# Optimization experiments

Measured on AMD Instinct MI355X. Metric: run time of the kernel, lower is better.

## Reference

```python
import jax, jax.numpy as jnp
import numpy as np

B, S, D, V, MAXLEN, K = 1, 2048, 768, 32000, 2048, 3
EPS = 1.1920929e-07  # torch.finfo(float32).eps, nn.RMSNorm default


def _linear_init(key, fan_in, fan_out):
    kw, kb = jax.random.split(key)
    bound = 1.0 / np.sqrt(fan_in)
    w = jax.random.uniform(kw, (fan_in, fan_out), minval=-bound, maxval=bound, dtype=jnp.float32)
    b = jax.random.uniform(kb, (fan_out,), minval=-bound, maxval=bound, dtype=jnp.float32)
    return w, b


def setup_inputs() -> dict:
    key = jax.random.key(0)
    ks = jax.random.split(key, 12)
    x = jax.random.randint(ks[0], (B, S), 0, V, dtype=jnp.int64)
    embedding = jax.random.normal(ks[1], (V, D), dtype=jnp.float32)
    pos_emb = jax.random.normal(ks[2], (MAXLEN, D), dtype=jnp.float32)
    # conv1d weight (out, in, k) torch layout
    bound = 1.0 / np.sqrt(D * K)
    conv_w = jax.random.uniform(ks[3], (D, D, K), minval=-bound, maxval=bound, dtype=jnp.float32)
    conv_b = jax.random.uniform(ks[4], (D,), minval=-bound, maxval=bound, dtype=jnp.float32)
    wg1, bg1 = _linear_init(ks[5], D, D)
    wmv, bmv = _linear_init(ks[6], 2 * D, D)
    wmg, bmg = _linear_init(ks[7], 2 * D, D)
    wrg, brg = _linear_init(ks[8], 2 * D, D)
    whw, bhw = _linear_init(ks[9], D, D)
    rms_w = jnp.ones((D,), dtype=jnp.float32)
    wpred, bpred = _linear_init(ks[10], D, V)
    return dict(x=x, embedding=embedding, pos_emb=pos_emb, conv_w=conv_w, conv_b=conv_b,
                wg1=wg1, bg1=bg1, wmv=wmv, bmv=bmv, wmg=wmg, bmg=bmg,
                wrg=wrg, brg=brg, whw=whw, bhw=bhw, rms_w=rms_w, wpred=wpred, bpred=bpred)


def _rmsnorm(x, w):
    ms = jnp.mean(jnp.square(x), axis=-1, keepdims=True)
    return x * jax.lax.rsqrt(ms + EPS) * w


def _causal_conv(x, conv_w, conv_b):
    # x: [B,S,D] -> left-pad by K-1, conv1d, back to [B,S,D]
    xc = jnp.transpose(x, (0, 2, 1))  # [B,D,S]
    y = jax.lax.conv_general_dilated(
        xc, conv_w, window_strides=(1,), padding=[(K - 1, 0)],
        dimension_numbers=('NCH', 'OIH', 'NCH'))
    y = y + conv_b[None, :, None]
    return jnp.transpose(y, (0, 2, 1))


def reference(x, embedding, pos_emb, conv_w, conv_b, wg1, bg1, wmv, bmv, wmg, bmg,
              wrg, brg, whw, bhw, rms_w, wpred, bpred):
    seq_len = x.shape[1]
    h = embedding[x] + pos_emb[:seq_len][None, :, :]
    h = _causal_conv(h, conv_w, conv_b)
    nodes = h * jax.nn.sigmoid(h @ wg1 + bg1)
    # Hillis-Steele log-depth causal scan
    curr = nodes
    step = 1
    while step < seq_len:
        left = curr[:, :-step, :]
        right = curr[:, step:, :]
        comb = jnp.concatenate([left, right], axis=-1)
        val = comb @ wmv + bmv
        gate = jax.nn.sigmoid(comb @ wmg + bmg)
        merged = _rmsnorm(val * gate, rms_w)
        hg = jax.nn.sigmoid(right @ whw + bhw)
        merged = hg * merged + (1.0 - hg) * right
        rg = jax.nn.sigmoid(comb @ wrg + brg)
        merged = rg * merged + (1.0 - rg) * (left + right) * 0.5
        curr = curr.at[:, step:, :].set(merged)
        step *= 2
    return curr @ wpred + bpred
```

## Files before the change

kernel.cpp:

```cpp
#include <hip/hip_runtime.h>
#include <hip/hip_bf16.h>

typedef __attribute__((ext_vector_type(8))) short short8;
typedef __attribute__((ext_vector_type(4))) float floatx4;
typedef __hip_bfloat16 bf16_t;

#define DD 768

__device__ __forceinline__ float sigmoid_f(float x) { return 1.f / (1.f + __expf(-x)); }

__device__ __forceinline__ void gl2lds16(const void* g, void* l) {
  __builtin_amdgcn_global_load_lds((const __attribute__((address_space(1))) void*)g,
                                   (__attribute__((address_space(3))) void*)l, 16, 0, 0);
}

__global__ __launch_bounds__(512, 2) void gemm256(
    const bf16_t* __restrict__ A, int lda, int M,
    const bf16_t* __restrict__ Wt, int Kdim,
    int nRowT, int nColT,
    const float* __restrict__ bias,
    float* __restrict__ out, int N)
{
  __shared__ __attribute__((aligned(16))) unsigned char lds[163840];
  const int tid = threadIdx.x;
  const int wave = tid >> 6, lane = tid & 63;
  const int l15 = lane & 15, kq = lane >> 4;
  const int wm = wave >> 2, wn = wave & 3;

  const int nwg = gridDim.x;
  const int q8 = nwg >> 3, r8 = nwg & 7;
  const int xcd = blockIdx.x & 7, lin = blockIdx.x >> 3;
  const int wgid = (xcd < r8 ? xcd * (q8 + 1) : r8 * (q8 + 1) + (xcd - r8) * q8) + lin;
  const int rowt = wgid % nRowT, colt = wgid / nRowT;
  const int rowbase = rowt * 256, colbase = colt * 256;

  floatx4 acc[8][4] = {};
  const int nkt = Kdim >> 6;

  auto stageA = [&](int mh, int kt, int buf) {
    const int kbase = kt << 6;
    #pragma unroll
    for (int rr = 0; rr < 2; ++rr) {
      const int L = rr * 64 + wave * 8;
      const int lrow_base = (L >> 6) * 128 + mh * 64 + (L & 63);
      const int lrow = lrow_base + (lane >> 3);
      const int slotp = (lane & 7) ^ (lrow & 7);
      const int gr = min(rowbase + lrow, M - 1);
      gl2lds16(A + (size_t)gr * lda + kbase + slotp * 8,
               lds + buf * 32768 + lrow_base * 128);
    }
  };
  auto stageB = [&](int nh, int kt, int buf) {
    const int kbase = kt << 6;
    #pragma unroll
    for (int rr = 0; rr < 2; ++rr) {
      const int L = rr * 64 + wave * 8;
      const int lrow_base = (L >> 5) * 64 + nh * 32 + (L & 31);
      const int lrow = lrow_base + (lane >> 3);
      const int slotp = (lane & 7) ^ (lrow & 7);
      const int gn = colbase + lrow;
      gl2lds16(Wt + (size_t)gn * Kdim + kbase + slotp * 8,
               lds + 65536 + buf * 32768 + lrow_base * 128);
    }
  };

#define READ_A(av_, mh_) \
  _Pragma("unroll") for (int i = 0; i < 4; ++i) { \
    const int r_ = wm * 128 + (mh_) * 64 + i * 16 + l15; \
    _Pragma("unroll") for (int s = 0; s < 2; ++s) { \
      const int sl_ = (s * 4 + kq) ^ (r_ & 7); \
      av_[i][s] = *reinterpret_cast<const short8*>(Ab + r_ * 128 + sl_ * 16); } }

#define READ_B(bv_, nh_) \
  _Pragma("unroll") for (int j = 0; j < 2; ++j) { \
    const int r_ = wn * 64 + (nh_) * 32 + j * 16 + l15; \
    _Pragma("unroll") for (int s = 0; s < 2; ++s) { \
      const int sl_ = (s * 4 + kq) ^ (r_ & 7); \
      bv_[j][s] = *reinterpret_cast<const short8*>(Bb + r_ * 128 + sl_ * 16); } }

#define MFMA_Q(av_, bv_, mb_, nb_) \
  __builtin_amdgcn_s_setprio(1); \
  _Pragma("unroll") for (int i = 0; i < 4; ++i) \
    _Pragma("unroll") for (int j = 0; j < 2; ++j) \
      _Pragma("unroll") for (int s = 0; s < 2; ++s) \
        acc[(mb_) + i][(nb_) + j] = __builtin_amdgcn_mfma_f32_16x16x32_bf16( \
            av_[i][s], bv_[j][s], acc[(mb_) + i][(nb_) + j], 0, 0, 0); \
  __builtin_amdgcn_s_setprio(0);

  stageB(0, 0, 0); stageB(1, 0, 0);
  stageA(0, 0, 0); stageA(1, 0, 0);
  if (nkt > 1) { stageB(0, 1, 1); stageB(1, 1, 1); }

  short8 av0[4][2], av1[4][2], bv0[2][2], bv1[2][2];
  int curA = 0, curB = 0;
  for (int t = 0; t < nkt; ++t) {
    const bool hasA = (t + 1 < nkt), hasB = (t + 2 < nkt);
    const unsigned char* Ab = lds + curA * 32768;
    const unsigned char* Bb = lds + 65536 + curB * 32768;
    int tgtB = curB + 2; if (tgtB >= 3) tgtB -= 3;

    if (hasA) { asm volatile("s_waitcnt vmcnt(6)" ::: "memory"); }
    else      { asm volatile("s_waitcnt vmcnt(2)" ::: "memory"); }
    __builtin_amdgcn_s_barrier();
    READ_A(av0, 0)
    READ_B(bv0, 0)
    if (hasA) stageA(0, t + 1, curA ^ 1);
    MFMA_Q(av0, bv0, 0, 0)

    READ_B(bv1, 1)
    if (hasA) stageA(1, t + 1, curA ^ 1);
    MFMA_Q(av0, bv1, 0, 2)

    if (hasA) { asm volatile("s_waitcnt vmcnt(8)" ::: "memory"); }
    else      { asm volatile("s_waitcnt vmcnt(0)" ::: "memory"); }
    __builtin_amdgcn_s_barrier();
    READ_A(av1, 1)
    if (hasB) stageB(0, t + 2, tgtB);
    MFMA_Q(av1, bv0, 4, 0)

    if (hasB) stageB(1, t + 2, tgtB);
    MFMA_Q(av1, bv1, 4, 2)

    curA ^= 1; curB = (curB + 1 == 3) ? 0 : curB + 1;
  }
#undef READ_A
#undef READ_B
#undef MFMA_Q

  const int hi = lane >> 4;
  #pragma unroll
  for (int i = 0; i < 8; ++i)
    #pragma unroll
    for (int j = 0; j < 4; ++j) {
      const int c = colbase + wn * 64 + j * 16 + l15;
      const float bb = bias[c];
      #pragma unroll
      for (int rg = 0; rg < 4; ++rg) {
        const int r = rowbase + wm * 128 + i * 16 + hi * 4 + rg;
        if (r < M) out[(size_t)r * N + c] = acc[i][j][rg] + bb;
      }
    }
}

__global__ __launch_bounds__(256, 2) void gemm128(
    const bf16_t* __restrict__ A, int lda, int M, int nRowT,
    int s0, int s1, int s2,
    const bf16_t* __restrict__ Wt, int Kdim,
    const float* __restrict__ bias,
    float* __restrict__ out, int N,
    bf16_t* __restrict__ out_bf,
    const float* __restrict__ gate_other)
{
  __shared__ __attribute__((aligned(16))) unsigned char lds[65536];
  const int tid = threadIdx.x;
  const int wave = tid >> 6, lane = tid & 63;
  const int l15 = lane & 15, kq = lane >> 4;
  const int wm = wave >> 1, wn = wave & 1;

  const int nwg = gridDim.x;
  const int q8 = nwg >> 3, r8 = nwg & 7;
  const int xcd = blockIdx.x & 7, lin = blockIdx.x >> 3;
  const int wgid = (xcd < r8 ? xcd * (q8 + 1) : r8 * (q8 + 1) + (xcd - r8) * q8) + lin;
  const int rowt = wgid % nRowT, colt = wgid / nRowT;
  const int rowbase = rowt * 128, colbase = colt * 128;

  floatx4 acc[4][4] = {};
  const int nkt = Kdim >> 6;

  auto stage = [&](int kt, int buf) {
    const int kbase = kt << 6;
    const int chunk = kbase / 768;
    const int shift = (chunk == 0) ? s0 : ((chunk == 1) ? s1 : s2);
    const int csrc  = kbase - chunk * 768;
    #pragma unroll
    for (int q = 0; q < 4; ++q) {
      const int Lb  = q * 32 + wave * 8;
      const int row = Lb + (lane >> 3);
      const int slotp = (lane & 7) ^ (row & 7);
      const int gr = min(rowbase + row, M - 1) + shift;
      gl2lds16(A + (size_t)gr * lda + csrc + slotp * 8,
               lds + buf * 16384 + Lb * 128);
      const int gn = colbase + row;
      gl2lds16(Wt + (size_t)gn * Kdim + kbase + slotp * 8,
               lds + 32768 + buf * 16384 + Lb * 128);
    }
  };

  stage(0, 0);
  int cur = 0;
  for (int t = 0; t < nkt; ++t) {
    if (t + 1 < nkt) {
      stage(t + 1, cur ^ 1);
      asm volatile("s_waitcnt vmcnt(8)" ::: "memory");
    } else {
      asm volatile("s_waitcnt vmcnt(0)" ::: "memory");
    }
    __builtin_amdgcn_s_barrier();

    const unsigned char* Ab = lds + cur * 16384;
    const unsigned char* Bb = lds + 32768 + cur * 16384;
    short8 av[4][2], bv[4][2];
    #pragma unroll
    for (int i = 0; i < 4; ++i) {
      const int r = wm * 64 + i * 16 + l15;
      #pragma unroll
      for (int s = 0; s < 2; ++s) {
        const int sl = (s * 4 + kq) ^ (r & 7);
        av[i][s] = *reinterpret_cast<const short8*>(Ab + r * 128 + sl * 16);
      }
    }
    #pragma unroll
    for (int j = 0; j < 4; ++j) {
      const int r = wn * 64 + j * 16 + l15;
      #pragma unroll
      for (int s = 0; s < 2; ++s) {
        const int sl = (s * 4 + kq) ^ (r & 7);
        bv[j][s] = *reinterpret_cast<const short8*>(Bb + r * 128 + sl * 16);
      }
    }
    __builtin_amdgcn_s_setprio(1);
    #pragma unroll
    for (int i = 0; i < 4; ++i)
      #pragma unroll
      for (int j = 0; j < 4; ++j)
        #pragma unroll
        for (int s = 0; s < 2; ++s)
          acc[i][j] = __builtin_amdgcn_mfma_f32_16x16x32_bf16(
              av[i][s], bv[j][s], acc[i][j], 0, 0, 0);
    __builtin_amdgcn_s_setprio(0);
    asm volatile("s_waitcnt lgkmcnt(0)" ::: "memory");
    __builtin_amdgcn_s_barrier();
    cur ^= 1;
  }

  const int hi = lane >> 4;
  #pragma unroll
  for (int i = 0; i < 4; ++i)
    #pragma unroll
    for (int j = 0; j < 4; ++j) {
      const int c = colbase + wn * 64 + j * 16 + l15;
      const float bb = bias[c];
      #pragma unroll
      for (int rg = 0; rg < 4; ++rg) {
        const int r = rowbase + wm * 64 + i * 16 + hi * 4 + rg;
        if (r < M) {
          float v = acc[i][j][rg] + bb;
          if (gate_other) v = gate_other[(size_t)r * N + c] * sigmoid_f(v);
          if (out)    out[(size_t)r * N + c] = v;
          if (out_bf) out_bf[(size_t)r * N + c] = __float2bfloat16(v);
        }
      }
    }
}

__global__ void transpose_cvt(const float* __restrict__ in, bf16_t* __restrict__ out,
                              int in_ld, int out_ld)
{
  __shared__ float tile[32][33];
  const int n0 = blockIdx.x * 32, k0 = blockIdx.y * 32;
  const int tx = threadIdx.x, ty = threadIdx.y;
  #pragma unroll
  for (int yy = ty; yy < 32; yy += 8)
    tile[yy][tx] = in[(size_t)(k0 + yy) * in_ld + n0 + tx];
  __syncthreads();
  #pragma unroll
  for (int yy = ty; yy < 32; yy += 8)
    out[(size_t)(n0 + yy) * out_ld + k0 + tx] = __float2bfloat16(tile[tx][yy]);
}

__global__ void build_wct(const float* __restrict__ cw, bf16_t* __restrict__ wct) {
  const int idx = blockIdx.x * 256 + threadIdx.x;
  const int o = idx / 2304, c = idx - o * 2304;
  const int k = c / 768, i = c - k * 768;
  wct[idx] = __float2bfloat16(cw[o * 2304 + i * 3 + k]);
}

__global__ void build_bias(const float* __restrict__ bmv, const float* __restrict__ bmg,
                           const float* __restrict__ brg, const float* __restrict__ bhw,
                           float* __restrict__ out) {
  const int i = blockIdx.x * 256 + threadIdx.x;
  float v;
  if (i < 768) v = bmv[i];
  else if (i < 1536) v = bmg[i - 768];
  else if (i < 2304) v = brg[i - 1536];
  else v = bhw[i - 2304];
  out[i] = v;
}

__global__ void embed_k(const int* __restrict__ x, const float* __restrict__ emb,
                        const float* __restrict__ pos, bf16_t* __restrict__ hpad) {
  const int t = blockIdx.x, tid = threadIdx.x;
  int id = 0, tt = t - 2;
  if (t >= 2) id = x[tt];
  #pragma unroll
  for (int q = 0; q < 3; ++q) {
    const int d = tid + q * 256;
    float v = 0.f;
    if (t >= 2) v = emb[(size_t)id * DD + d] + pos[(size_t)tt * DD + d];
    hpad[(size_t)t * DD + d] = __float2bfloat16(v);
  }
}

__global__ __launch_bounds__(256) void merge_ew(
    const bf16_t* __restrict__ curOldB, const float* __restrict__ curOldF,
    bf16_t* __restrict__ curNewB, float* __restrict__ curNewF,
    const bf16_t* __restrict__ tmp,
    const float* __restrict__ rmsw, int step)
{
  const int t = blockIdx.x, tid = threadIdx.x;
  if (t < step) {
    const uint4* sF = (const uint4*)(curOldF + (size_t)t * DD);
    uint4* dF = (uint4*)(curNewF + (size_t)t * DD);
    if (tid < 192) dF[tid] = sF[tid];
    const uint4* sB = (const uint4*)(curOldB + (size_t)t * DD);
    uint4* dB = (uint4*)(curNewB + (size_t)t * DD);
    if (tid < 96) dB[tid] = sB[tid];
    return;
  }
  const int r = t - step;
  const bf16_t* row = tmp + (size_t)r * 3072;
  float mv[3]; float ss = 0.f;
  #pragma unroll
  for (int q = 0; q < 3; ++q) {
    const int d = tid + q * 256;
    const float m = __bfloat162float(row[d]) * sigmoid_f(__bfloat162float(row[768 + d]));
    mv[q] = m; ss += m * m;
  }
  #pragma unroll
  for (int o = 32; o >= 1; o >>= 1) ss += __shfl_down(ss, o, 64);
  __shared__ float red[4];
  if ((tid & 63) == 0) red[tid >> 6] = ss;
  __syncthreads();
  const float tot = red[0] + red[1] + red[2] + red[3];
  const float scale = rsqrtf(tot * (1.f / 768.f) + 1.1920929e-07f);
  #pragma unroll
  for (int q = 0; q < 3; ++q) {
    const int d = tid + q * 256;
    float merged = mv[q] * scale * rmsw[d];
    const float right = curOldF[(size_t)t * DD + d];
    const float left  = curOldF[(size_t)r * DD + d];
    const float hg = sigmoid_f(__bfloat162float(row[2304 + d]));
    merged = hg * merged + (1.f - hg) * right;
    const float rg = sigmoid_f(__bfloat162float(row[1536 + d]));
    merged = rg * merged + (1.f - rg) * (left + right) * 0.5f;
    curNewF[(size_t)t * DD + d] = merged;
    curNewB[(size_t)t * DD + d] = __float2bfloat16(merged);
  }
}

extern "C" void kernel_launch(void* const* d_in, const int* in_sizes, int n_in,
                              void* d_out, int out_size, void* d_ws, size_t ws_size,
                              hipStream_t stream) {
  const int*   x      = (const int*)  d_in[0];
  const float* emb    = (const float*)d_in[1];
  const float* pos    = (const float*)d_in[2];
  const float* conv_w = (const float*)d_in[3];
  const float* conv_b = (const float*)d_in[4];
  const float* wg1    = (const float*)d_in[5];
  const float* bg1    = (const float*)d_in[6];
  const float* wmv    = (const float*)d_in[7];
  const float* bmv    = (const float*)d_in[8];
  const float* wmg    = (const float*)d_in[9];
  const float* bmg    = (const float*)d_in[10];
  const float* wrg    = (const float*)d_in[11];
  const float* brg    = (const float*)d_in[12];
  const float* whw    = (const float*)d_in[13];
  const float* bhw    = (const float*)d_in[14];
  const float* rmsw   = (const float*)d_in[15];
  const float* wpred  = (const float*)d_in[16];
  const float* bpred  = (const float*)d_in[17];

  char* ws = (char*)d_ws;
  size_t off = 0;
  auto carve = [&](size_t bytes) { char* p = ws + off; off += (bytes + 255) & ~(size_t)255; return p; };
  bf16_t* wpred_t  = (bf16_t*)carve(32000ull * 768 * 2);
  bf16_t* Wbig_t   = (bf16_t*)carve(3072ull * 1536 * 2);
  bf16_t* wc_t     = (bf16_t*)carve(768ull * 2304 * 2);
  bf16_t* wg1_t    = (bf16_t*)carve(768ull * 768 * 2);
  float*  bias_big = (float*) carve(3072 * 4);
  bf16_t* h_pad    = (bf16_t*)carve(2050ull * 768 * 2);
  float*  hconv    = (float*) carve(2048ull * 768 * 4);
  bf16_t* hconv_bf = (bf16_t*)carve(2048ull * 768 * 2);
  bf16_t* currA_b  = (bf16_t*)carve(2048ull * 768 * 2);
  bf16_t* currB_b  = (bf16_t*)carve(2048ull * 768 * 2);
  float*  currA_f  = (float*) carve(2048ull * 768 * 4);
  float*  currB_f  = (float*) carve(2048ull * 768 * 4);
  bf16_t* tmp_bf   = (bf16_t*)carve(2048ull * 3072 * 2);

  const dim3 tb(32, 8);
  hipMemsetAsync(Wbig_t + 2304ull * 1536, 0, 768ull * 1536 * 2, stream);
  transpose_cvt<<<dim3(24, 48), tb, 0, stream>>>(wmv, Wbig_t,                        768, 1536);
  transpose_cvt<<<dim3(24, 48), tb, 0, stream>>>(wmg, Wbig_t + 768ull * 1536,        768, 1536);
  transpose_cvt<<<dim3(24, 48), tb, 0, stream>>>(wrg, Wbig_t + 1536ull * 1536,       768, 1536);
  transpose_cvt<<<dim3(24, 24), tb, 0, stream>>>(whw, Wbig_t + 2304ull * 1536 + 768, 768, 1536);
  transpose_cvt<<<dim3(24, 24), tb, 0, stream>>>(wg1, wg1_t, 768, 768);
  transpose_cvt<<<dim3(1000, 24), tb, 0, stream>>>(wpred, wpred_t, 32000, 768);
  build_wct<<<6912, 256, 0, stream>>>(conv_w, wc_t);
  build_bias<<<12, 256, 0, stream>>>(bmv, bmg, brg, bhw, bias_big);

  embed_k<<<2050, 256, 0, stream>>>(x, emb, pos, h_pad);

  gemm128<<<16 * 6, 256, 0, stream>>>(h_pad, 768, 2048, 16, 0, 1, 2,
                                      wc_t, 2304, conv_b, hconv, 768, hconv_bf, nullptr);
  gemm128<<<16 * 6, 256, 0, stream>>>(hconv_bf, 768, 2048, 16, 0, 0, 0,
                                      wg1_t, 768, bg1, currA_f, 768, currA_b, hconv);

  bf16_t* curB = currA_b; float* curF = currA_f;
  bf16_t* nxtB = currB_b; float* nxtF = currB_f;
  for (int step = 1; step < 2048; step <<= 1) {
    const int M = 2048 - step;
    const int nRowT = (M + 127) / 128;
    gemm128<<<nRowT * 24, 256, 0, stream>>>(
        curB, 768, M, nRowT, 0, step, 0, Wbig_t, 1536, bias_big,
        nullptr, 3072, tmp_bf, nullptr);
    merge_ew<<<2048, 256, 0, stream>>>(curB, curF, nxtB, nxtF, tmp_bf, rmsw, step);
    { bf16_t* tb_ = curB; curB = nxtB; nxtB = tb_; }
    { float*  tf_ = curF; curF = nxtF; nxtF = tf_; }
  }

  gemm256<<<8 * 125, 512, 0, stream>>>(curB, 768, 2048, wpred_t, 768, 8, 125,
                                       bpred, (float*)d_out, 32000);
}
```

Baseline: 739.4 us.

## Switch GEMM kernels to BK=32 multi-stage LDS pipelines with single barrier

Both GEMM kernels now use a K-tile of 32 instead of 64. gemm256 moves to a 4-buffer ring with three tiles prefetched, and gemm128 to a 3-buffer ring with two tiles prefetched. Each iteration needs one barrier with a staged vmcnt wait, and the swizzle is changed to 4 slots. The goal is deeper load/compute overlap, fewer barriers per tile, and lower LDS use, which lets gemm128 run 3 blocks per CU (launch bounds changed to 3). In exchange, each barrier covers fewer MFMAs and the K loop has twice as many iterations.

Result: slower. 820.9 us (+11.0%).

```diff
diff --git a/kernel.cpp b/kernel.cpp
--- a/kernel.cpp
+++ b/kernel.cpp
@@ -13,6 +13,7 @@
   __builtin_amdgcn_global_load_lds((const __attribute__((address_space(1))) void*)g,
                                    (__attribute__((address_space(3))) void*)l, 16, 0, 0);
 }
+
 
 __global__ __launch_bounds__(512, 2) void gemm256(
     const bf16_t* __restrict__ A, int lda, int M,
@@ -21,7 +22,7 @@
     const float* __restrict__ bias,
     float* __restrict__ out, int N)
 {
-  __shared__ __attribute__((aligned(16))) unsigned char lds[163840];
+  __shared__ __attribute__((aligned(16))) unsigned char lds[131072];
   const int tid = threadIdx.x;
   const int wave = tid >> 6, lane = tid & 63;
   const int l15 = lane & 15, kq = lane >> 4;
@@ -35,97 +36,59 @@
   const int rowbase = rowt * 256, colbase = colt * 256;
 
   floatx4 acc[8][4] = {};
-  const int nkt = Kdim >> 6;
-
-  auto stageA = [&](int mh, int kt, int buf) {
-    const int kbase = kt << 6;
+  const int nkt = Kdim >> 5;
+
+  auto stage = [&](int kt, int buf) {
+    const int kbase = kt << 5;
     #pragma unroll
     for (int rr = 0; rr < 2; ++rr) {
-      const int L = rr * 64 + wave * 8;
-      const int lrow_base = (L >> 6) * 128 + mh * 64 + (L & 63);
-      const int lrow = lrow_base + (lane >> 3);
-      const int slotp = (lane & 7) ^ (lrow & 7);
-      const int gr = min(rowbase + lrow, M - 1);
-      gl2lds16(A + (size_t)gr * lda + kbase + slotp * 8,
-               lds + buf * 32768 + lrow_base * 128);
+      const int L = wave * 32 + rr * 16;
+      const int row = L + (lane >> 2);
+      const int sl = (lane & 3) ^ (row & 3);
+      const int gr = min(rowbase + row, M - 1);
+      gl2lds16(A + (size_t)gr * lda + kbase + sl * 8,
+               lds + buf * 16384 + L * 64);
+      const int gn = colbase + row;
+      gl2lds16(Wt + (size_t)gn * Kdim + kbase + sl * 8,
+               lds + 65536 + buf * 16384 + L * 64);
     }
   };
-  auto stageB = [&](int nh, int kt, int buf) {
-    const int kbase = kt << 6;
-    #pragma unroll
-    for (int rr = 0; rr < 2; ++rr) {
-      const int L = rr * 64 + wave * 8;
-      const int lrow_base = (L >> 5) * 64 + nh * 32 + (L & 31);
-      const int lrow = lrow_base + (lane >> 3);
-      const int slotp = (lane & 7) ^ (lrow & 7);
-      const int gn = colbase + lrow;
-      gl2lds16(Wt + (size_t)gn * Kdim + kbase + slotp * 8,
-               lds + 65536 + buf * 32768 + lrow_base * 128);
-    }
-  };
-
-#define READ_A(av_, mh_) \
-  _Pragma("unroll") for (int i = 0; i < 4; ++i) { \
-    const int r_ = wm * 128 + (mh_) * 64 + i * 16 + l15; \
-    _Pragma("unroll") for (int s = 0; s < 2; ++s) { \
-      const int sl_ = (s * 4 + kq) ^ (r_ & 7); \
-      av_[i][s] = *reinterpret_cast<const short8*>(Ab + r_ * 128 + sl_ * 16); } }
-
-#define READ_B(bv_, nh_) \
-  _Pragma("unroll") for (int j = 0; j < 2; ++j) { \
-    const int r_ = wn * 64 + (nh_) * 32 + j * 16 + l15; \
-    _Pragma("unroll") for (int s = 0; s < 2; ++s) { \
-      const int sl_ = (s * 4 + kq) ^ (r_ & 7); \
-      bv_[j][s] = *reinterpret_cast<const short8*>(Bb + r_ * 128 + sl_ * 16); } }
-
-#define MFMA_Q(av_, bv_, mb_, nb_) \
-  __builtin_amdgcn_s_setprio(1); \
-  _Pragma("unroll") for (int i = 0; i < 4; ++i) \
-    _Pragma("unroll") for (int j = 0; j < 2; ++j) \
-      _Pragma("unroll") for (int s = 0; s < 2; ++s) \
-        acc[(mb_) + i][(nb_) + j] = __builtin_amdgcn_mfma_f32_16x16x32_bf16( \
-            av_[i][s], bv_[j][s], acc[(mb_) + i][(nb_) + j], 0, 0, 0); \
-  __builtin_amdgcn_s_setprio(0);
-
-  stageB(0, 0, 0); stageB(1, 0, 0);
-  stageA(0, 0, 0); stageA(1, 0, 0);
-  if (nkt > 1) { stageB(0, 1, 1); stageB(1, 1, 1); }
-
-  short8 av0[4][2], av1[4][2], bv0[2][2], bv1[2][2];
-  int curA = 0, curB = 0;
+
+  stage(0, 0); stage(1, 1); stage(2, 2);
+  asm volatile("s_waitcnt vmcnt(8)" ::: "memory");
+  __builtin_amdgcn_s_barrier();
+  __builtin_amdgcn_sched_barrier(0);
+
   for (int t = 0; t < nkt; ++t) {
-    const bool hasA = (t + 1 < nkt), hasB = (t + 2 < nkt);
-    const unsigned char* Ab = lds + curA * 32768;
-    const unsigned char* Bb = lds + 65536 + curB * 32768;
-    int tgtB = curB + 2; if (tgtB >= 3) tgtB -= 3;
-
-    if (hasA) { asm volatile("s_waitcnt vmcnt(6)" ::: "memory"); }
-    else      { asm volatile("s_waitcnt vmcnt(2)" ::: "memory"); }
-    __builtin_amdgcn_s_barrier();
-    READ_A(av0, 0)
-    READ_B(bv0, 0)
-    if (hasA) stageA(0, t + 1, curA ^ 1);
-    MFMA_Q(av0, bv0, 0, 0)
-
-    READ_B(bv1, 1)
-    if (hasA) stageA(1, t + 1, curA ^ 1);
-    MFMA_Q(av0, bv1, 0, 2)
-
-    if (hasA) { asm volatile("s_waitcnt vmcnt(8)" ::: "memory"); }
-    else      { asm volatile("s_waitcnt vmcnt(0)" ::: "memory"); }
-    __builtin_amdgcn_s_barrier();
-    READ_A(av1, 1)
-    if (hasB) stageB(0, t + 2, tgtB);
-    MFMA_Q(av1, bv0, 4, 0)
-
-    if (hasB) stageB(1, t + 2, tgtB);
-    MFMA_Q(av1, bv1, 4, 2)
-
-    curA ^= 1; curB = (curB + 1 == 3) ? 0 : curB + 1;
-  }
-#undef READ_A
-#undef READ_B
-#undef MFMA_Q
+    if (t + 3 < nkt) stage(t + 3, (t + 3) & 3);
+    const unsigned char* Ab = lds + (t & 3) * 16384;
+    const unsigned char* Bb = lds + 65536 + (t & 3) * 16384;
+    short8 av[8], bv[4];
+    #pragma unroll
+    for (int i = 0; i < 8; ++i) {
+      const int r = wm * 128 + i * 16 + l15;
+      av[i] = *reinterpret_cast<const short8*>(Ab + r * 64 + ((kq ^ (r & 3)) << 4));
+    }
+    #pragma unroll
+    for (int j = 0; j < 4; ++j) {
+      const int r = wn * 64 + j * 16 + l15;
+      bv[j] = *reinterpret_cast<const short8*>(Bb + r * 64 + ((kq ^ (r & 3)) << 4));
+    }
+    __builtin_amdgcn_s_setprio(1);
+    #pragma unroll
+    for (int i = 0; i < 8; ++i)
+      #pragma unroll
+      for (int j = 0; j < 4; ++j)
+        acc[i][j] = __builtin_amdgcn_mfma_f32_16x16x32_bf16(av[i], bv[j], acc[i][j], 0, 0, 0);
+    __builtin_amdgcn_s_setprio(0);
+    if (t + 1 < nkt) {
+      if (t + 3 < nkt)      { asm volatile("s_waitcnt vmcnt(8)" ::: "memory"); }
+      else if (t + 2 < nkt) { asm volatile("s_waitcnt vmcnt(4)" ::: "memory"); }
+      else                  { asm volatile("s_waitcnt vmcnt(0)" ::: "memory"); }
+      __builtin_amdgcn_s_barrier();
+      __builtin_amdgcn_sched_barrier(0);
+    }
+  }
 
   const int hi = lane >> 4;
   #pragma unroll
@@ -142,7 +105,7 @@
     }
 }
 
-__global__ __launch_bounds__(256, 2) void gemm128(
+__global__ __launch_bounds__(256, 3) void gemm128(
     const bf16_t* __restrict__ A, int lda, int M, int nRowT,
     int s0, int s1, int s2,
     const bf16_t* __restrict__ Wt, int Kdim,
@@ -151,7 +114,7 @@
     bf16_t* __restrict__ out_bf,
     const float* __restrict__ gate_other)
 {
-  __shared__ __attribute__((aligned(16))) unsigned char lds[65536];
+  __shared__ __attribute__((aligned(16))) unsigned char lds[49152];
   const int tid = threadIdx.x;
   const int wave = tid >> 6, lane = tid & 63;
   const int l15 = lane & 15, kq = lane >> 4;
@@ -165,72 +128,66 @@
   const int rowbase = rowt * 128, colbase = colt * 128;
 
   floatx4 acc[4][4] = {};
-  const int nkt = Kdim >> 6;
+  const int nkt = Kdim >> 5;
 
   auto stage = [&](int kt, int buf) {
-    const int kbase = kt << 6;
+    const int kbase = kt << 5;
     const int chunk = kbase / 768;
     const int shift = (chunk == 0) ? s0 : ((chunk == 1) ? s1 : s2);
     const int csrc  = kbase - chunk * 768;
     #pragma unroll
-    for (int q = 0; q < 4; ++q) {
-      const int Lb  = q * 32 + wave * 8;
-      const int row = Lb + (lane >> 3);
-      const int slotp = (lane & 7) ^ (row & 7);
+    for (int rr = 0; rr < 2; ++rr) {
+      const int L = wave * 32 + rr * 16;
+      const int row = L + (lane >> 2);
+      const int sl = (lane & 3) ^ (row & 3);
       const int gr = min(rowbase + row, M - 1) + shift;
-      gl2lds16(A + (size_t)gr * lda + csrc + slotp * 8,
-               lds + buf * 16384 + Lb * 128);
+      gl2lds16(A + (size_t)gr * lda + csrc + sl * 8,
+               lds + buf * 8192 + L * 64);
       const int gn = colbase + row;
-      gl2lds16(Wt + (size_t)gn * Kdim + kbase + slotp * 8,
-               lds + 32768 + buf * 16384 + Lb * 128);
+      gl2lds16(Wt + (size_t)gn * Kdim + kbase + sl * 8,
+               lds + 24576 + buf * 8192 + L * 64);
     }
   };
 
   stage(0, 0);
-  int cur = 0;
+  if (nkt > 1) {
+    stage(1, 1);
+    asm volatile("s_waitcnt vmcnt(4)" ::: "memory");
+  } else {
+    asm volatile("s_waitcnt vmcnt(0)" ::: "memory");
+  }
+  __builtin_amdgcn_s_barrier();
+  __builtin_amdgcn_sched_barrier(0);
+
   for (int t = 0; t < nkt; ++t) {
-    if (t + 1 < nkt) {
-      stage(t + 1, cur ^ 1);
-      asm volatile("s_waitcnt vmcnt(8)" ::: "memory");
-    } else {
-      asm volatile("s_waitcnt vmcnt(0)" ::: "memory");
-    }
-    __builtin_amdgcn_s_barrier();
-
-    const unsigned char* Ab = lds + cur * 16384;
-    const unsigned char* Bb = lds + 32768 + cur * 16384;
-    short8 av[4][2], bv[4][2];
+    if (t + 2 < nkt) { int b = t + 2; while (b >= 3) b -= 3; stage(t + 2, b); }
+    int cb = t; while (cb >= 3) cb -= 3;
+    const unsigned char* Ab = lds + cb * 8192;
+    const unsigned char* Bb = lds + 24576 + cb * 8192;
+    short8 av[4], bv[4];
     #pragma unroll
     for (int i = 0; i < 4; ++i) {
       const int r = wm * 64 + i * 16 + l15;
-      #pragma unroll
-      for (int s = 0; s < 2; ++s) {
-        const int sl = (s * 4 + kq) ^ (r & 7);
-        av[i][s] = *reinterpret_cast<const short8*>(Ab + r * 128 + sl * 16);
-      }
+      av[i] = *reinterpret_cast<const short8*>(Ab + r * 64 + ((kq ^ (r & 3)) << 4));
     }
     #pragma unroll
     for (int j = 0; j < 4; ++j) {
       const int r = wn * 64 + j * 16 + l15;
-      #pragma unroll
-      for (int s = 0; s < 2; ++s) {
-        const int sl = (s * 4 + kq) ^ (r & 7);
-        bv[j][s] = *reinterpret_cast<const short8*>(Bb + r * 128 + sl * 16);
-      }
+      bv[j] = *reinterpret_cast<const short8*>(Bb + r * 64 + ((kq ^ (r & 3)) << 4));
     }
     __builtin_amdgcn_s_setprio(1);
     #pragma unroll
     for (int i = 0; i < 4; ++i)
       #pragma unroll
       for (int j = 0; j < 4; ++j)
-        #pragma unroll
-        for (int s = 0; s < 2; ++s)
-          acc[i][j] = __builtin_amdgcn_mfma_f32_16x16x32_bf16(
-              av[i][s], bv[j][s], acc[i][j], 0, 0, 0);
+        acc[i][j] = __builtin_amdgcn_mfma_f32_16x16x32_bf16(av[i], bv[j], acc[i][j], 0, 0, 0);
     __builtin_amdgcn_s_setprio(0);
-    asm volatile("s_waitcnt lgkmcnt(0)" ::: "memory");
-    __builtin_amdgcn_s_barrier();
-    cur ^= 1;
+    if (t + 1 < nkt) {
+      if (t + 2 < nkt) { asm volatile("s_waitcnt vmcnt(4)" ::: "memory"); }
+      else             { asm volatile("s_waitcnt vmcnt(0)" ::: "memory"); }
+      __builtin_amdgcn_s_barrier();
+      __builtin_amdgcn_sched_barrier(0);
+    }
   }
 
   const int hi = lane >> 4;
```
